# Optimization experiments

Measured on AMD Instinct MI355X. Metric: run time of the kernel, lower is better.

Reference implementation:

```python
import jax, jax.numpy as jnp
import numpy as np

B, C, H, W = 8, 512, 56, 56
CI = C // 2  # inter_channels
EPS = 1e-5   # BatchNorm eps


def setup_inputs() -> dict:
    key = jax.random.key(0)
    ks = jax.random.split(key, 11)
    s = 0.02
    return {
        "x": jax.random.normal(ks[0], (B, C, H, W), jnp.float32),
        "theta_w": jax.random.normal(ks[1], (CI, C), jnp.float32) * s,
        "theta_b": jnp.zeros((CI,), jnp.float32),
        "phi_w": jax.random.normal(ks[2], (CI, C), jnp.float32) * s,
        "phi_b": jnp.zeros((CI,), jnp.float32),
        "g_w": jax.random.normal(ks[3], (CI, C), jnp.float32) * s,
        "g_b": jnp.zeros((CI,), jnp.float32),
        "w_w": jax.random.normal(ks[4], (C, CI), jnp.float32) * s,
        "w_b": jnp.zeros((C,), jnp.float32),
        "bn_gamma": jax.random.normal(ks[5], (C,), jnp.float32) * 0.1,
        "bn_beta": jax.random.normal(ks[6], (C,), jnp.float32) * 0.1,
    }


def reference(x, theta_w, theta_b, phi_w, phi_b, g_w, g_b, w_w, w_b, bn_gamma, bn_beta):
    b, c, h, w = x.shape
    n = h * w

    def proj(wt, bi):  # 1x1 conv -> [b, out, n]
        return (jnp.einsum('bchw,oc->bohw', x, wt) + bi[None, :, None, None]).reshape(b, -1, n)

    theta_x = proj(theta_w, theta_b).transpose(0, 2, 1)  # [b, n, ci]
    phi_x = proj(phi_w, phi_b)                           # [b, ci, n]
    g_x = proj(g_w, g_b).transpose(0, 2, 1)             # [b, n, ci]

    f = jnp.einsum('bnc,bcm->bnm', theta_x, phi_x)       # [b, n, n] unscaled scores
    f_div_c = jax.nn.softmax(f, axis=-1)
    y = jnp.einsum('bnm,bmc->bnc', f_div_c, g_x)         # [b, n, ci]
    y = y.transpose(0, 2, 1).reshape(b, -1, h, w)        # [b, ci, h, w]

    w_y = jnp.einsum('bchw,oc->bohw', y, w_w) + w_b[None, :, None, None]
    # BatchNorm2d (training mode, batch statistics over B,H,W per channel)
    mean = w_y.mean(axis=(0, 2, 3))
    var = w_y.var(axis=(0, 2, 3))
    w_y = (w_y - mean[None, :, None, None]) * jax.lax.rsqrt(var[None, :, None, None] + EPS)
    w_y = w_y * bn_gamma[None, :, None, None] + bn_beta[None, :, None, None]
    return w_y + x
```

## Files before the change

### kernel.cpp

```cpp
#include <hip/hip_runtime.h>
#include <hip/hip_bf16.h>


typedef unsigned short u16;
typedef unsigned int u32;
typedef __attribute__((ext_vector_type(8))) short short8;
typedef __attribute__((ext_vector_type(4))) float floatx4;

#define B_   8
#define C_   512
#define CI_  256
#define N_   3136
#define BN_  25088

__device__ __forceinline__ u16 f2b(float f) {
    return __builtin_bit_cast(u16, __float2bfloat16(f));
}
__device__ __forceinline__ float b2f(u16 u) {
    return __bfloat162float(__builtin_bit_cast(__hip_bfloat16, u));
}
__device__ __forceinline__ floatx4 mfma16(short8 a, short8 b, floatx4 c) {
    return __builtin_amdgcn_mfma_f32_16x16x32_bf16(a, b, c, 0, 0, 0);
}
__device__ __forceinline__ void gload_lds16(const u16* g, u16* l) {
    __builtin_amdgcn_global_load_lds(
        (const __attribute__((address_space(1))) u32*)g,
        (__attribute__((address_space(3))) u32*)l, 16, 0, 0);
}

__global__ void detect_dtype(const u32* __restrict__ xw, int* __restrict__ flag,
                             float* __restrict__ stats)
{
    __shared__ int cnt;
    if (threadIdx.x == 0) cnt = 0;
    __syncthreads();
    int c = 0;
    for (int i = 0; i < 16; ++i) {
        u32 w = xw[threadIdx.x * 16 + i];
        u32 e = (w >> 7) & 0xFF;
        c += (e >= 118 && e <= 130) ? 1 : 0;
    }
    atomicAdd(&cnt, c);
    stats[threadIdx.x] = 0.f;
    stats[threadIdx.x + 256] = 0.f;
    stats[threadIdx.x + 512] = 0.f;
    stats[threadIdx.x + 768] = 0.f;
    __syncthreads();
    if (threadIdx.x == 0) *flag = (2 * cnt > 4096) ? 1 : 0;
}

__global__ __launch_bounds__(256) void convert_params(
    const void* tw, const void* tb, const void* pw, const void* pb,
    const void* gw, const void* gbi, const void* ww, const void* wb,
    const void* gamma, const void* beta,
    u16* __restrict__ dst, const int* __restrict__ flag)
{
    const void* srcs[10] = {tw, tb, pw, pb, gw, gbi, ww, wb, gamma, beta};
    const int ns[10] = {131072, 256, 131072, 256, 131072, 256, 131072, 512, 512, 512};
    int seg = blockIdx.y;
    int off = 0;
    for (int s = 0; s < 10; ++s) { if (s == seg) break; off += ns[s]; }
    const void* src = srcs[seg];
    int n = ns[seg];
    int i0 = (blockIdx.x * 256 + threadIdx.x) * 8;
    if (i0 >= n) return;
    const int fl = *flag;
    u16* d = dst + off;
    for (int k = 0; k < 8; ++k) {
        int i = i0 + k;
        if (i < n)
            d[i] = fl ? ((const u16*)src)[i] : f2b(((const float*)src)[i]);
    }
}

__global__ __launch_bounds__(256) void transpose_x(
    const void* __restrict__ in, u16* __restrict__ out,
    const int* __restrict__ flag)
{
    __shared__ u16 tile[64][68];
    const int fl = *flag;
    const int t = threadIdx.x;
    const long base = (long)blockIdx.z * (long)C_ * (long)N_;
    const int c0 = blockIdx.x * 64, r0 = blockIdx.y * 64;
    const int lr = t >> 3;
    const int lc = (t & 7) * 8;
#pragma unroll
    for (int j = 0; j < 2; ++j) {
        int rr = lr + 32 * j;
        long eoff = base + (long)(r0 + rr) * N_ + c0 + lc;
        u16 v[8] __attribute__((aligned(16)));
        if (fl) {
            const u16* pi = (const u16*)in + eoff;
            *(uint64_t*)&v[0] = *(const uint64_t*)pi;
            *(uint64_t*)&v[4] = *(const uint64_t*)(pi + 4);
        } else {
            const float* pi = (const float*)in + eoff;
            floatx4 a = *(const floatx4*)pi;
            floatx4 b4 = *(const floatx4*)(pi + 4);
#pragma unroll
            for (int k = 0; k < 4; ++k) { v[k] = f2b(a[k]); v[4 + k] = f2b(b4[k]); }
        }
        *(uint64_t*)&tile[rr][lc] = *(const uint64_t*)&v[0];
        *(uint64_t*)&tile[rr][lc + 4] = *(const uint64_t*)&v[4];
    }
    __syncthreads();
#pragma unroll
    for (int j = 0; j < 2; ++j) {
        int oc = lr + 32 * j;
        int ob = (t & 7) * 8;
        u16 vals[8] __attribute__((aligned(16)));
#pragma unroll
        for (int k = 0; k < 8; ++k) vals[k] = tile[ob + k][oc];
        u16* po = out + (long)blockIdx.z * N_ * C_ + (long)(c0 + oc) * C_ + r0 + ob;
        *(uint64_t*)po = *(const uint64_t*)vals;
        *(uint64_t*)(po + 4) = *(const uint64_t*)(vals + 4);
    }
}

__global__ __launch_bounds__(256) void transpose64(
    const u16* __restrict__ in, u16* __restrict__ out, int R, int Cc)
{
    __shared__ u16 tile[64][68];
    const int t = threadIdx.x;
    const long base = (long)blockIdx.z * (long)R * (long)Cc;
    const int c0 = blockIdx.x * 64, r0 = blockIdx.y * 64;
    const int lr = t >> 3;
    const int lc = (t & 7) * 8;
#pragma unroll
    for (int j = 0; j < 2; ++j) {
        int rr = lr + 32 * j;
        const u16* pi = in + base + (long)(r0 + rr) * Cc + c0 + lc;
        *(uint64_t*)&tile[rr][lc] = *(const uint64_t*)pi;
        *(uint64_t*)&tile[rr][lc + 4] = *(const uint64_t*)(pi + 4);
    }
    __syncthreads();
#pragma unroll
    for (int j = 0; j < 2; ++j) {
        int oc = lr + 32 * j;
        int ob = (t & 7) * 8;
        u16 vals[8] __attribute__((aligned(16)));
#pragma unroll
        for (int k = 0; k < 8; ++k) vals[k] = tile[ob + k][oc];
        u16* po = out + base + (long)(c0 + oc) * R + r0 + ob;
        *(uint64_t*)po = *(const uint64_t*)vals;
        *(uint64_t*)(po + 4) = *(const uint64_t*)(vals + 4);
    }
}

template<int K>
__global__ __launch_bounds__(256, 3) void gemm128(
    const u16* __restrict__ A,
    const u16* __restrict__ BtBase,
    const u16* __restrict__ biasBase,
    u16* __restrict__ OutBase,
    int ncols, long bstride, long ostride)
{
    __shared__ __attribute__((aligned(16))) u16 Asf[2][8][64][8];
    __shared__ __attribute__((aligned(16))) u16 Bsf[2][8][64][8];

    const int t = threadIdx.x;
    const int wave = t >> 6, lane = t & 63;
    const int q = lane >> 4, lx = lane & 15;
    const int m0 = blockIdx.x * 128;
    const int n0 = blockIdx.y * 128;
    const u16* Bt = BtBase + (long)blockIdx.z * bstride;
    const u16* bias = biasBase + (long)blockIdx.z * bstride;
    u16* Out = OutBase + (long)blockIdx.z * ostride;

    floatx4 zero4 = {0.f, 0.f, 0.f, 0.f};
    floatx4 acc[4][4];
#pragma unroll
    for (int i = 0; i < 4; ++i)
#pragma unroll
        for (int j = 0; j < 4; ++j) acc[i][j] = zero4;

    auto stage = [&](int buf, int k0) {
#pragma unroll
        for (int i = 0; i < 2; ++i) {
            int rg = wave * 2 + i;
            gload_lds16(A + (long)(m0 + rg * 16 + lx) * K + k0 + q * 8,
                        &Asf[buf][rg][0][0]);
            gload_lds16(Bt + (long)(n0 + rg * 16 + lx) * K + k0 + q * 8,
                        &Bsf[buf][rg][0][0]);
        }
    };

    stage(0, 0);
    const int rg0 = (wave >> 1) * 4, cg0 = (wave & 1) * 4;
    const int NS = K / 32;
    for (int s = 0; s < NS; ++s) {
        const int buf = s & 1;
        __syncthreads();
        if (s + 1 < NS) stage(buf ^ 1, (s + 1) * 32);
        short8 af[4], bfr[4];
#pragma unroll
        for (int i = 0; i < 4; ++i)
            af[i] = *(const short8*)&Asf[buf][rg0 + i][lane][0];
#pragma unroll
        for (int j = 0; j < 4; ++j)
            bfr[j] = *(const short8*)&Bsf[buf][cg0 + j][lane][0];
#pragma unroll
        for (int i = 0; i < 4; ++i)
#pragma unroll
            for (int j = 0; j < 4; ++j)
                acc[i][j] = mfma16(af[i], bfr[j], acc[i][j]);
    }

    const int wr = (wave >> 1) * 64, wc = (wave & 1) * 64;
#pragma unroll
    for (int j = 0; j < 4; ++j) {
        int col = n0 + wc + j * 16 + lx;
        float bv = b2f(bias[col]);
#pragma unroll
        for (int i = 0; i < 4; ++i) {
#pragma unroll
            for (int r = 0; r < 4; ++r) {
                int row = m0 + wr + i * 16 + q * 4 + r;
                Out[(long)row * ncols + col] = f2b(acc[i][j][r] + bv);
            }
        }
    }
}

__global__ __launch_bounds__(256, 2) void attn(
    const u16* __restrict__ theta,
    const u16* __restrict__ phi,
    const u16* __restrict__ gT,
    u16* __restrict__ yp0, u16* __restrict__ yp1,
    u16* __restrict__ yp2, u16* __restrict__ yp3,
    float* __restrict__ lpart)
{
    __shared__ __attribute__((aligned(16))) u16 psf[2][8][2][64][8];
    __shared__ __attribute__((aligned(16))) u16 gsf[2][16][64][8];
    __shared__ __attribute__((aligned(16))) u16 Ps[4][32][40];

    const int t = threadIdx.x;
    const int wave = t >> 6, lane = t & 63;
    const int q = lane >> 4, lx = lane & 15;
    const int b = blockIdx.y;
    const int z = blockIdx.z;
    const int n0w = blockIdx.x * 128 + wave * 32;
    const bool valid = n0w < N_;
    const u16* thb = theta + (long)b * N_ * CI_;
    const u16* phb = phi + (long)b * N_ * CI_;
    const u16* gb = gT + (long)b * CI_ * N_;

    short8 tf[2][8];
#pragma unroll
    for (int h = 0; h < 2; ++h) {
        int trow = n0w + h * 16 + lx;
        if (trow >= N_) trow = N_ - 1;
#pragma unroll
        for (int kk = 0; kk < 8; ++kk)
            tf[h][kk] = *(const short8*)(thb + (long)trow * CI_ + kk * 32 + q * 8);
    }

    floatx4 zero4 = {0.f, 0.f, 0.f, 0.f};
    floatx4 yacc[2][16];
#pragma unroll
    for (int h = 0; h < 2; ++h)
#pragma unroll
        for (int i = 0; i < 16; ++i) yacc[h][i] = zero4;
    floatx4 lacc[2] = {zero4, zero4};
    const short8 ones = {0x3F80, 0x3F80, 0x3F80, 0x3F80,
                         0x3F80, 0x3F80, 0x3F80, 0x3F80};

    const int mbeg = z * 800;
    const int mend = (z == 3) ? N_ : mbeg + 800;

    auto stage = [&](int buf, int m0) {
#pragma unroll
        for (int i = 0; i < 2; ++i) {
            int kc = wave * 2 + i;
#pragma unroll
            for (int h = 0; h < 2; ++h)
                gload_lds16(phb + (long)(m0 + h * 16 + lx) * CI_ + kc * 32 + q * 8,
                            &psf[buf][kc][h][0][0]);
        }
#pragma unroll
        for (int j4 = 0; j4 < 4; ++j4) {
            int ct = wave * 4 + j4;
            gload_lds16(gb + (long)(ct * 16 + lx) * N_ + m0 + q * 8,
                        &gsf[buf][ct][0][0]);
        }
    };

    stage(0, mbeg);
    const int NSTEP = (mend - mbeg) / 32;
    for (int s = 0; s < NSTEP; ++s) {
        const int buf = s & 1;
        __syncthreads();
        if (s + 1 < NSTEP) stage(buf ^ 1, mbeg + (s + 1) * 32);

        floatx4 sacc[2][2];
        sacc[0][0] = zero4; sacc[0][1] = zero4;
        sacc[1][0] = zero4; sacc[1][1] = zero4;
#pragma unroll
        for (int kk = 0; kk < 8; ++kk) {
            short8 bf0 = *(const short8*)&psf[buf][kk][0][lane][0];
            short8 bf1 = *(const short8*)&psf[buf][kk][1][lane][0];
            sacc[0][0] = mfma16(tf[0][kk], bf0, sacc[0][0]);
            sacc[1][0] = mfma16(tf[1][kk], bf0, sacc[1][0]);
            sacc[0][1] = mfma16(tf[0][kk], bf1, sacc[0][1]);
            sacc[1][1] = mfma16(tf[1][kk], bf1, sacc[1][1]);
        }

#pragma unroll
        for (int h = 0; h < 2; ++h)
#pragma unroll
            for (int mh = 0; mh < 2; ++mh)
#pragma unroll
                for (int r = 0; r < 4; ++r) {
                    float e = __expf(fminf(sacc[h][mh][r], 60.f));
                    Ps[wave][h * 16 + q * 4 + r][mh * 16 + lx] = f2b(e);
                }
        short8 gpre[4];
#pragma unroll
        for (int j = 0; j < 4; ++j)
            gpre[j] = *(const short8*)&gsf[buf][j][lane][0];
        __builtin_amdgcn_wave_barrier();
        short8 pA0 = *(const short8*)&Ps[wave][lx][q * 8];
        short8 pA1 = *(const short8*)&Ps[wave][16 + lx][q * 8];
        __builtin_amdgcn_wave_barrier();

#pragma unroll
        for (int j = 0; j < 4; ++j) {
            yacc[0][j] = mfma16(pA0, gpre[j], yacc[0][j]);
            yacc[1][j] = mfma16(pA1, gpre[j], yacc[1][j]);
        }
#pragma unroll
        for (int ct = 4; ct < 16; ++ct) {
            short8 gf = *(const short8*)&gsf[buf][ct][lane][0];
            yacc[0][ct] = mfma16(pA0, gf, yacc[0][ct]);
            yacc[1][ct] = mfma16(pA1, gf, yacc[1][ct]);
        }
        lacc[0] = mfma16(pA0, ones, lacc[0]);
        lacc[1] = mfma16(pA1, ones, lacc[1]);
    }

    if (valid) {
        u16* ypz = (z == 0) ? yp0 : (z == 1) ? yp1 : (z == 2) ? yp2 : yp3;
        u16* yb = ypz + (long)b * N_ * CI_;
#pragma unroll
        for (int h = 0; h < 2; ++h)
#pragma unroll
            for (int ct = 0; ct < 16; ++ct)
#pragma unroll
                for (int r = 0; r < 4; ++r)
                    yb[(long)(n0w + h * 16 + q * 4 + r) * CI_ + ct * 16 + lx] =
                        f2b(yacc[h][ct][r]);
        if (lx == 0) {
#pragma unroll
            for (int h = 0; h < 2; ++h)
#pragma unroll
                for (int r = 0; r < 4; ++r)
                    lpart[(long)z * BN_ + (long)b * N_ + n0w + h * 16 + q * 4 + r] =
                        lacc[h][r];
        }
    }
}

__global__ __launch_bounds__(256) void attn_combine(
    const u16* __restrict__ yp0, const u16* __restrict__ yp1,
    const u16* __restrict__ yp2, const u16* __restrict__ yp3,
    const float* __restrict__ lpart, u16* __restrict__ y)
{
    long tt = (long)blockIdx.x * 256 + threadIdx.x;
    long row = tt >> 5;
    int cb = (int)(tt & 31) * 8;
    float l = lpart[row] + lpart[BN_ + row] + lpart[2 * BN_ + row]
            + lpart[3 * BN_ + row];
    float rl = 1.0f / l;
    long off = row * CI_ + cb;
    short8 v0 = *(const short8*)(yp0 + off);
    short8 v1 = *(const short8*)(yp1 + off);
    short8 v2 = *(const short8*)(yp2 + off);
    short8 v3 = *(const short8*)(yp3 + off);
    u16 ov[8] __attribute__((aligned(16)));
#pragma unroll
    for (int j = 0; j < 8; ++j)
        ov[j] = f2b((b2f(((const u16*)&v0)[j]) + b2f(((const u16*)&v1)[j]) +
                     b2f(((const u16*)&v2)[j]) + b2f(((const u16*)&v3)[j])) * rl);
    *(short8*)(y + off) = *(const short8*)ov;
}

__global__ __launch_bounds__(256) void bn_stats(
    const u16* __restrict__ wy, float* __restrict__ stats)
{
    const int t = threadIdx.x;
    const long row0 = (long)blockIdx.x * 32;
    float s0 = 0.f, s1 = 0.f, q0 = 0.f, q1 = 0.f;
    for (int r = 0; r < 32; ++r) {
        const u16* p = wy + (row0 + r) * C_;
        float a = b2f(p[t]), b = b2f(p[t + 256]);
        s0 += a; q0 += a * a;
        s1 += b; q1 += b * b;
    }
    atomicAdd(&stats[t], s0);
    atomicAdd(&stats[t + 256], s1);
    atomicAdd(&stats[C_ + t], q0);
    atomicAdd(&stats[C_ + t + 256], q1);
}

__global__ __launch_bounds__(256) void bn_apply(
    const u16* __restrict__ wy, const void* __restrict__ xv,
    const u16* __restrict__ gamma, const u16* __restrict__ beta,
    const float* __restrict__ stats, void* __restrict__ outv,
    const int* __restrict__ flag)
{
    __shared__ float tile[64][65];
    const int fl = *flag;
    const int t = threadIdx.x;
    const int nb0 = blockIdx.x * 64;
    const int c0 = blockIdx.y * 64;
    const int b = blockIdx.z;
#pragma unroll
    for (int j = 0; j < 4; ++j) {
        int row = (t >> 4) + 16 * j;
        int col = (t & 15) * 4;
        const u16* p = wy + ((long)b * N_ + nb0 + row) * C_ + c0 + col;
        u16 lv[4] __attribute__((aligned(8)));
        *(uint64_t*)lv = *(const uint64_t*)p;
#pragma unroll
        for (int k = 0; k < 4; ++k) tile[row][col + k] = b2f(lv[k]);
    }
    __syncthreads();
    const float inv = 1.0f / (float)BN_;
#pragma unroll
    for (int it = 0; it < 8; ++it) {
        int oc = (t >> 5) + 8 * it;
        int on = (t & 31) * 2;
        int c = c0 + oc;
        float mean = stats[c] * inv;
        float var = stats[C_ + c] * inv - mean * mean;
        float rstd = rsqrtf(var + 1e-5f);
        float sc = b2f(gamma[c]) * rstd;
        float sh = b2f(beta[c]) - mean * sc;
        long base = ((long)b * C_ + c) * N_ + nb0 + on;
        float v0 = tile[on][oc] * sc + sh;
        float v1 = tile[on + 1][oc] * sc + sh;
        if (fl) {
            v0 += b2f(((const u16*)xv)[base]);
            v1 += b2f(((const u16*)xv)[base + 1]);
            ((u16*)outv)[base] = f2b(v0);
            ((u16*)outv)[base + 1] = f2b(v1);
        } else {
            v0 += ((const float*)xv)[base];
            v1 += ((const float*)xv)[base + 1];
            ((float*)outv)[base] = v0;
            ((float*)outv)[base + 1] = v1;
        }
    }
}

extern "C" void kernel_launch(void* const* d_in, const int* in_sizes, int n_in,
                              void* d_out, int out_size, void* d_ws, size_t ws_size,
                              hipStream_t stream)
{
    (void)in_sizes; (void)n_in; (void)out_size; (void)ws_size;

    const size_t S = 12845056;
    const size_t SE = S / 2;
    char* base = (char*)d_ws;
    u16*   xT    = (u16*)(base);
    u16*   gT    = (u16*)(base);
    u16*   y     = (u16*)(base + S);
    u16*   th    = (u16*)(base + 2 * S);
    u16*   wy    = (u16*)(base + 2 * S);
    u16*   gn    = (u16*)(base + 4 * S);
    float* lpart = (float*)(base + 5 * S);
    float* stats = (float*)(base + 5 * S + (size_t)4 * BN_ * 4);
    u16*   cw    = (u16*)(base + 5 * S + (size_t)4 * BN_ * 4 + 4096);
    int*   flag  = (int*)(base + 5 * S + (size_t)4 * BN_ * 4 + 4096 + 1055744);

    u16* ctw = cw;               u16* ctb = cw + 131072;
    u16* cww = ctb + 256 + 2 * 131328;  u16* cwb = cww + 131072;
    u16* cga = cwb + 512;        u16* cbe = cga + 512;

    u16* yp0 = (u16*)d_out;
    u16* yp1 = (u16*)d_out + SE;
    u16* yp2 = y;
    u16* yp3 = gn;

    detect_dtype<<<1, 256, 0, stream>>>((const u32*)d_in[0], flag, stats);
    convert_params<<<dim3(64, 10), 256, 0, stream>>>(
        d_in[1], d_in[2], d_in[3], d_in[4], d_in[5], d_in[6], d_in[7],
        d_in[8], d_in[9], d_in[10], cw, flag);

    transpose_x<<<dim3(N_ / 64, C_ / 64, B_), 256, 0, stream>>>(d_in[0], xT, flag);

    gemm128<C_><<<dim3(BN_ / 128, CI_ / 128, 3), 256, 0, stream>>>(
        xT, ctw, ctb, th, CI_, 131328L, (long)SE);

    transpose64<<<dim3(CI_ / 64, N_ / 64, B_), 256, 0, stream>>>(gn, gT, N_, CI_);

    attn<<<dim3(25, B_, 4), 256, 0, stream>>>(
        th, th + SE, gT, yp0, yp1, yp2, yp3, lpart);

    attn_combine<<<dim3((BN_ * 32) / 256), 256, 0, stream>>>(
        yp0, yp1, yp2, yp3, lpart, y);

    gemm128<CI_><<<dim3(BN_ / 128, C_ / 128, 1), 256, 0, stream>>>(
        y, cww, cwb, wy, C_, 0L, 0L);

    bn_stats<<<BN_ / 32, 256, 0, stream>>>(wy, stats);

    bn_apply<<<dim3(N_ / 64, C_ / 64, B_), 256, 0, stream>>>(
        wy, d_in[0], cga, cbe, stats, d_out, flag);
}
```

Before: 387.1 us.

## Fuse transpose, attention combine, and BN stats into neighbouring GEMMs; drop flag kernel

Removes the separate dtype-detect kernel by having each kernel compute the dtype flag locally from a small sample of x. Fuses the g transpose into the projection GEMM epilogue through LDS, and fuses the split-attention combine (sum of partials times 1/l) into the A-operand load of the output-projection GEMM. The batch-norm statistics are now accumulated in that GEMM's epilogue with shuffles and atomics. This cuts four kernel launches and several full-tensor round trips through memory, at the cost of register-staged A loads in gemm_w and redundant flag sampling in every block.

```diff
diff --git a/kernel.cpp b/kernel.cpp
--- a/kernel.cpp
+++ b/kernel.cpp
@@ -28,33 +28,37 @@
         (__attribute__((address_space(3))) u32*)l, 16, 0, 0);
 }
 
-__global__ void detect_dtype(const u32* __restrict__ xw, int* __restrict__ flag,
-                             float* __restrict__ stats)
-{
-    __shared__ int cnt;
-    if (threadIdx.x == 0) cnt = 0;
+__device__ __forceinline__ int block_flag(const void* x) {
+    __shared__ int cnt_;
+    if (threadIdx.x == 0) cnt_ = 0;
     __syncthreads();
+    const u32* xw = (const u32*)x;
     int c = 0;
-    for (int i = 0; i < 16; ++i) {
-        u32 w = xw[threadIdx.x * 16 + i];
+#pragma unroll
+    for (int i = 0; i < 4; ++i) {
+        u32 w = xw[threadIdx.x * 4 + i];
         u32 e = (w >> 7) & 0xFF;
         c += (e >= 118 && e <= 130) ? 1 : 0;
     }
-    atomicAdd(&cnt, c);
-    stats[threadIdx.x] = 0.f;
-    stats[threadIdx.x + 256] = 0.f;
-    stats[threadIdx.x + 512] = 0.f;
-    stats[threadIdx.x + 768] = 0.f;
+    atomicAdd(&cnt_, c);
     __syncthreads();
-    if (threadIdx.x == 0) *flag = (2 * cnt > 4096) ? 1 : 0;
+    return (2 * cnt_ > 1024) ? 1 : 0;
 }
 
 __global__ __launch_bounds__(256) void convert_params(
+    const void* __restrict__ x,
     const void* tw, const void* tb, const void* pw, const void* pb,
     const void* gw, const void* gbi, const void* ww, const void* wb,
     const void* gamma, const void* beta,
-    u16* __restrict__ dst, const int* __restrict__ flag)
-{
+    u16* __restrict__ dst, float* __restrict__ stats)
+{
+    const int fl = block_flag(x);
+    if (blockIdx.x == 0 && blockIdx.y == 0) {
+        stats[threadIdx.x] = 0.f;
+        stats[threadIdx.x + 256] = 0.f;
+        stats[threadIdx.x + 512] = 0.f;
+        stats[threadIdx.x + 768] = 0.f;
+    }
     const void* srcs[10] = {tw, tb, pw, pb, gw, gbi, ww, wb, gamma, beta};
     const int ns[10] = {131072, 256, 131072, 256, 131072, 256, 131072, 512, 512, 512};
     int seg = blockIdx.y;
@@ -64,7 +68,6 @@
     int n = ns[seg];
     int i0 = (blockIdx.x * 256 + threadIdx.x) * 8;
     if (i0 >= n) return;
-    const int fl = *flag;
     u16* d = dst + off;
     for (int k = 0; k < 8; ++k) {
         int i = i0 + k;
@@ -74,11 +77,10 @@
 }
 
 __global__ __launch_bounds__(256) void transpose_x(
-    const void* __restrict__ in, u16* __restrict__ out,
-    const int* __restrict__ flag)
-{
+    const void* __restrict__ in, u16* __restrict__ out)
+{
+    const int fl = block_flag(in);
     __shared__ u16 tile[64][68];
-    const int fl = *flag;
     const int t = threadIdx.x;
     const long base = (long)blockIdx.z * (long)C_ * (long)N_;
     const int c0 = blockIdx.x * 64, r0 = blockIdx.y * 64;
@@ -117,55 +119,25 @@
     }
 }
 
-__global__ __launch_bounds__(256) void transpose64(
-    const u16* __restrict__ in, u16* __restrict__ out, int R, int Cc)
-{
-    __shared__ u16 tile[64][68];
-    const int t = threadIdx.x;
-    const long base = (long)blockIdx.z * (long)R * (long)Cc;
-    const int c0 = blockIdx.x * 64, r0 = blockIdx.y * 64;
-    const int lr = t >> 3;
-    const int lc = (t & 7) * 8;
-#pragma unroll
-    for (int j = 0; j < 2; ++j) {
-        int rr = lr + 32 * j;
-        const u16* pi = in + base + (long)(r0 + rr) * Cc + c0 + lc;
-        *(uint64_t*)&tile[rr][lc] = *(const uint64_t*)pi;
-        *(uint64_t*)&tile[rr][lc + 4] = *(const uint64_t*)(pi + 4);
-    }
-    __syncthreads();
-#pragma unroll
-    for (int j = 0; j < 2; ++j) {
-        int oc = lr + 32 * j;
-        int ob = (t & 7) * 8;
-        u16 vals[8] __attribute__((aligned(16)));
-#pragma unroll
-        for (int k = 0; k < 8; ++k) vals[k] = tile[ob + k][oc];
-        u16* po = out + base + (long)(c0 + oc) * R + r0 + ob;
-        *(uint64_t*)po = *(const uint64_t*)vals;
-        *(uint64_t*)(po + 4) = *(const uint64_t*)(vals + 4);
-    }
-}
-
-template<int K>
-__global__ __launch_bounds__(256, 3) void gemm128(
+__global__ __launch_bounds__(256, 3) void gemm_proj(
     const u16* __restrict__ A,
     const u16* __restrict__ BtBase,
-    const u16* __restrict__ biasBase,
     u16* __restrict__ OutBase,
-    int ncols, long bstride, long ostride)
-{
-    __shared__ __attribute__((aligned(16))) u16 Asf[2][8][64][8];
-    __shared__ __attribute__((aligned(16))) u16 Bsf[2][8][64][8];
-
+    u16* __restrict__ gT,
+    long ostride)
+{
+    __shared__ __attribute__((aligned(16))) u16 smem[16896];
     const int t = threadIdx.x;
     const int wave = t >> 6, lane = t & 63;
     const int q = lane >> 4, lx = lane & 15;
     const int m0 = blockIdx.x * 128;
     const int n0 = blockIdx.y * 128;
-    const u16* Bt = BtBase + (long)blockIdx.z * bstride;
-    const u16* bias = biasBase + (long)blockIdx.z * bstride;
-    u16* Out = OutBase + (long)blockIdx.z * ostride;
+    const int zz = blockIdx.z;
+    const u16* Bt = BtBase + (long)zz * 131328L;
+    const u16* bias = Bt + 131072;
+
+    auto As = [&](int buf, int rg) -> u16* { return smem + (buf * 8 + rg) * 512; };
+    auto Bs = [&](int buf, int rg) -> u16* { return smem + 8192 + (buf * 8 + rg) * 512; };
 
     floatx4 zero4 = {0.f, 0.f, 0.f, 0.f};
     floatx4 acc[4][4];
@@ -178,27 +150,24 @@
 #pragma unroll
         for (int i = 0; i < 2; ++i) {
             int rg = wave * 2 + i;
-            gload_lds16(A + (long)(m0 + rg * 16 + lx) * K + k0 + q * 8,
-                        &Asf[buf][rg][0][0]);
-            gload_lds16(Bt + (long)(n0 + rg * 16 + lx) * K + k0 + q * 8,
-                        &Bsf[buf][rg][0][0]);
+            gload_lds16(A + (long)(m0 + rg * 16 + lx) * C_ + k0 + q * 8, As(buf, rg));
+            gload_lds16(Bt + (long)(n0 + rg * 16 + lx) * C_ + k0 + q * 8, Bs(buf, rg));
         }
     };
 
     stage(0, 0);
     const int rg0 = (wave >> 1) * 4, cg0 = (wave & 1) * 4;
-    const int NS = K / 32;
-    for (int s = 0; s < NS; ++s) {
+    for (int s = 0; s < C_ / 32; ++s) {
         const int buf = s & 1;
         __syncthreads();
-        if (s + 1 < NS) stage(buf ^ 1, (s + 1) * 32);
+        if (s + 1 < C_ / 32) stage(buf ^ 1, (s + 1) * 32);
         short8 af[4], bfr[4];
 #pragma unroll
         for (int i = 0; i < 4; ++i)
-            af[i] = *(const short8*)&Asf[buf][rg0 + i][lane][0];
+            af[i] = *(const short8*)(As(buf, rg0 + i) + lane * 8);
 #pragma unroll
         for (int j = 0; j < 4; ++j)
-            bfr[j] = *(const short8*)&Bsf[buf][cg0 + j][lane][0];
+            bfr[j] = *(const short8*)(Bs(buf, cg0 + j) + lane * 8);
 #pragma unroll
         for (int i = 0; i < 4; ++i)
 #pragma unroll
@@ -207,17 +176,47 @@
     }
 
     const int wr = (wave >> 1) * 64, wc = (wave & 1) * 64;
-#pragma unroll
-    for (int j = 0; j < 4; ++j) {
-        int col = n0 + wc + j * 16 + lx;
-        float bv = b2f(bias[col]);
-#pragma unroll
-        for (int i = 0; i < 4; ++i) {
-#pragma unroll
-            for (int r = 0; r < 4; ++r) {
-                int row = m0 + wr + i * 16 + q * 4 + r;
-                Out[(long)row * ncols + col] = f2b(acc[i][j][r] + bv);
-            }
+    if (zz < 2) {
+        u16* Out = OutBase + (long)zz * ostride;
+#pragma unroll
+        for (int j = 0; j < 4; ++j) {
+            int col = n0 + wc + j * 16 + lx;
+            float bv = b2f(bias[col]);
+#pragma unroll
+            for (int i = 0; i < 4; ++i)
+#pragma unroll
+                for (int r = 0; r < 4; ++r) {
+                    int row = m0 + wr + i * 16 + q * 4 + r;
+                    Out[(long)row * CI_ + col] = f2b(acc[i][j][r] + bv);
+                }
+        }
+    } else {
+        __syncthreads();
+#pragma unroll
+        for (int j = 0; j < 4; ++j) {
+            int cl = wc + j * 16 + lx;
+            float bv = b2f(bias[n0 + cl]);
+#pragma unroll
+            for (int i = 0; i < 4; ++i)
+#pragma unroll
+                for (int r = 0; r < 4; ++r)
+                    smem[cl * 132 + wr + i * 16 + q * 4 + r] =
+                        f2b(acc[i][j][r] + bv);
+        }
+        __syncthreads();
+#pragma unroll
+        for (int p = 0; p < 4; ++p) {
+            int cc = (t >> 3) + p * 32;
+            int nn0 = (t & 7) * 16;
+            u16 vals[16] __attribute__((aligned(16)));
+#pragma unroll
+            for (int k = 0; k < 16; ++k) vals[k] = smem[cc * 132 + nn0 + k];
+            int m = m0 + nn0;
+            int bb = m / N_;
+            int nn = m - bb * N_;
+            u16* dst = gT + ((long)bb * CI_ + (n0 + cc)) * N_ + nn;
+            *(short8*)dst = *(const short8*)&vals[0];
+            *(short8*)(dst + 8) = *(const short8*)&vals[8];
         }
     }
 }
@@ -360,56 +359,127 @@
     }
 }
 
-__global__ __launch_bounds__(256) void attn_combine(
+__global__ __launch_bounds__(256, 3) void gemm_w(
     const u16* __restrict__ yp0, const u16* __restrict__ yp1,
     const u16* __restrict__ yp2, const u16* __restrict__ yp3,
-    const float* __restrict__ lpart, u16* __restrict__ y)
-{
-    long tt = (long)blockIdx.x * 256 + threadIdx.x;
-    long row = tt >> 5;
-    int cb = (int)(tt & 31) * 8;
-    float l = lpart[row] + lpart[BN_ + row] + lpart[2 * BN_ + row]
-            + lpart[3 * BN_ + row];
-    float rl = 1.0f / l;
-    long off = row * CI_ + cb;
-    short8 v0 = *(const short8*)(yp0 + off);
-    short8 v1 = *(const short8*)(yp1 + off);
-    short8 v2 = *(const short8*)(yp2 + off);
-    short8 v3 = *(const short8*)(yp3 + off);
-    u16 ov[8] __attribute__((aligned(16)));
-#pragma unroll
-    for (int j = 0; j < 8; ++j)
-        ov[j] = f2b((b2f(((const u16*)&v0)[j]) + b2f(((const u16*)&v1)[j]) +
-                     b2f(((const u16*)&v2)[j]) + b2f(((const u16*)&v3)[j])) * rl);
-    *(short8*)(y + off) = *(const short8*)ov;
-}
-
-__global__ __launch_bounds__(256) void bn_stats(
-    const u16* __restrict__ wy, float* __restrict__ stats)
-{
+    const float* __restrict__ lpart,
+    const u16* __restrict__ Bt,
+    const u16* __restrict__ bias,
+    u16* __restrict__ wy,
+    float* __restrict__ stats)
+{
+    __shared__ __attribute__((aligned(16))) u16 Asf[2][8][64][8];
+    __shared__ __attribute__((aligned(16))) u16 Bsf[2][8][64][8];
+
     const int t = threadIdx.x;
-    const long row0 = (long)blockIdx.x * 32;
-    float s0 = 0.f, s1 = 0.f, q0 = 0.f, q1 = 0.f;
-    for (int r = 0; r < 32; ++r) {
-        const u16* p = wy + (row0 + r) * C_;
-        float a = b2f(p[t]), b = b2f(p[t + 256]);
-        s0 += a; q0 += a * a;
-        s1 += b; q1 += b * b;
-    }
-    atomicAdd(&stats[t], s0);
-    atomicAdd(&stats[t + 256], s1);
-    atomicAdd(&stats[C_ + t], q0);
-    atomicAdd(&stats[C_ + t + 256], q1);
+    const int wave = t >> 6, lane = t & 63;
+    const int q = lane >> 4, lx = lane & 15;
+    const int m0 = blockIdx.x * 128;
+    const int n0 = blockIdx.y * 128;
+
+    float rl[2];
+#pragma unroll
+    for (int i = 0; i < 2; ++i) {
+        int row = m0 + (wave * 2 + i) * 16 + lx;
+        rl[i] = 1.0f / (lpart[row] + lpart[BN_ + row] +
+                        lpart[2 * BN_ + row] + lpart[3 * BN_ + row]);
+    }
+
+    floatx4 zero4 = {0.f, 0.f, 0.f, 0.f};
+    floatx4 acc[4][4];
+#pragma unroll
+    for (int i = 0; i < 4; ++i)
+#pragma unroll
+        for (int j = 0; j < 4; ++j) acc[i][j] = zero4;
+
+    short8 va[2][4];
+    auto loadA = [&](int k0) {
+#pragma unroll
+        for (int i = 0; i < 2; ++i) {
+            long off = (long)(m0 + (wave * 2 + i) * 16 + lx) * CI_ + k0 + q * 8;
+            va[i][0] = *(const short8*)(yp0 + off);
+            va[i][1] = *(const short8*)(yp1 + off);
+            va[i][2] = *(const short8*)(yp2 + off);
+            va[i][3] = *(const short8*)(yp3 + off);
+        }
+    };
+    auto writeA = [&](int buf) {
+#pragma unroll
+        for (int i = 0; i < 2; ++i) {
+            u16 pk[8] __attribute__((aligned(16)));
+#pragma unroll
+            for (int e = 0; e < 8; ++e) {
+                float v = (b2f(((const u16*)&va[i][0])[e]) +
+                           b2f(((const u16*)&va[i][1])[e]) +
+                           b2f(((const u16*)&va[i][2])[e]) +
+                           b2f(((const u16*)&va[i][3])[e])) * rl[i];
+                pk[e] = f2b(v);
+            }
+            *(short8*)&Asf[buf][wave * 2 + i][lane][0] = *(const short8*)pk;
+        }
+    };
+    auto stageB = [&](int buf, int k0) {
+#pragma unroll
+        for (int i = 0; i < 2; ++i) {
+            int rg = wave * 2 + i;
+            gload_lds16(Bt + (long)(n0 + rg * 16 + lx) * CI_ + k0 + q * 8,
+                        &Bsf[buf][rg][0][0]);
+        }
+    };
+
+    loadA(0); writeA(0); stageB(0, 0);
+    const int rg0 = (wave >> 1) * 4, cg0 = (wave & 1) * 4;
+    const int NS = CI_ / 32;
+    for (int s = 0; s < NS; ++s) {
+        const int buf = s & 1;
+        __syncthreads();
+        if (s + 1 < NS) { loadA((s + 1) * 32); stageB(buf ^ 1, (s + 1) * 32); }
+        short8 af[4], bfr[4];
+#pragma unroll
+        for (int i = 0; i < 4; ++i)
+            af[i] = *(const short8*)&Asf[buf][rg0 + i][lane][0];
+#pragma unroll
+        for (int j = 0; j < 4; ++j)
+            bfr[j] = *(const short8*)&Bsf[buf][cg0 + j][lane][0];
+#pragma unroll
+        for (int i = 0; i < 4; ++i)
+#pragma unroll
+            for (int j = 0; j < 4; ++j)
+                acc[i][j] = mfma16(af[i], bfr[j], acc[i][j]);
+        if (s + 1 < NS) writeA(buf ^ 1);
+    }
+
+    const int wr = (wave >> 1) * 64, wc = (wave & 1) * 64;
+#pragma unroll
+    for (int j = 0; j < 4; ++j) {
+        int col = n0 + wc + j * 16 + lx;
+        float bv = b2f(bias[col]);
+        float cs = 0.f, cq = 0.f;
+#pragma unroll
+        for (int i = 0; i < 4; ++i)
+#pragma unroll
+            for (int r = 0; r < 4; ++r) {
+                int row = m0 + wr + i * 16 + q * 4 + r;
+                float v = acc[i][j][r] + bv;
+                wy[(long)row * C_ + col] = f2b(v);
+                cs += v; cq += v * v;
+            }
+        cs += __shfl_xor(cs, 16); cs += __shfl_xor(cs, 32);
+        cq += __shfl_xor(cq, 16); cq += __shfl_xor(cq, 32);
+        if (q == 0) {
+            atomicAdd(&stats[col], cs);
+            atomicAdd(&stats[C_ + col], cq);
+        }
+    }
 }
 
 __global__ __launch_bounds__(256) void bn_apply(
     const u16* __restrict__ wy, const void* __restrict__ xv,
     const u16* __restrict__ gamma, const u16* __restrict__ beta,
-    const float* __restrict__ stats, void* __restrict__ outv,
-    const int* __restrict__ flag)
-{
+    const float* __restrict__ stats, void* __restrict__ outv)
+{
+    const int fl = block_flag(xv);
     __shared__ float tile[64][65];
-    const int fl = *flag;
     const int t = threadIdx.x;
     const int nb0 = blockIdx.x * 64;
     const int c0 = blockIdx.y * 64;
@@ -463,48 +533,39 @@
     const size_t SE = S / 2;
     char* base = (char*)d_ws;
     u16*   xT    = (u16*)(base);
-    u16*   gT    = (u16*)(base);
-    u16*   y     = (u16*)(base + S);
+    u16*   yp3   = (u16*)(base);
+    u16*   yp2   = (u16*)(base + S);
     u16*   th    = (u16*)(base + 2 * S);
     u16*   wy    = (u16*)(base + 2 * S);
-    u16*   gn    = (u16*)(base + 4 * S);
+    u16*   gT    = (u16*)(base + 4 * S);
     float* lpart = (float*)(base + 5 * S);
     float* stats = (float*)(base + 5 * S + (size_t)4 * BN_ * 4);
     u16*   cw    = (u16*)(base + 5 * S + (size_t)4 * BN_ * 4 + 4096);
-    int*   flag  = (int*)(base + 5 * S + (size_t)4 * BN_ * 4 + 4096 + 1055744);
-
-    u16* ctw = cw;               u16* ctb = cw + 131072;
-    u16* cww = ctb + 256 + 2 * 131328;  u16* cwb = cww + 131072;
-    u16* cga = cwb + 512;        u16* cbe = cga + 512;
+
+    u16* ctw = cw;
+    u16* cww = cw + 393984;
+    u16* cwb = cw + 525056;
+    u16* cga = cw + 525568;
+    u16* cbe = cw + 526080;
 
     u16* yp0 = (u16*)d_out;
     u16* yp1 = (u16*)d_out + SE;
-    u16* yp2 = y;
-    u16* yp3 = gn;
-
-    detect_dtype<<<1, 256, 0, stream>>>((const u32*)d_in[0], flag, stats);
+
     convert_params<<<dim3(64, 10), 256, 0, stream>>>(
-        d_in[1], d_in[2], d_in[3], d_in[4], d_in[5], d_in[6], d_in[7],
-        d_in[8], d_in[9], d_in[10], cw, flag);
-
-    transpose_x<<<dim3(N_ / 64, C_ / 64, B_), 256, 0, stream>>>(d_in[0], xT, flag);
-
-    gemm128<C_><<<dim3(BN_ / 128, CI_ / 128, 3), 256, 0, stream>>>(
-        xT, ctw, ctb, th, CI_, 131328L, (long)SE);
-
-    transpose64<<<dim3(CI_ / 64, N_ / 64, B_), 256, 0, stream>>>(gn, gT, N_, CI_);
+        d_in[0], d_in[1], d_in[2], d_in[3], d_in[4], d_in[5], d_in[6],
+        d_in[7], d_in[8], d_in[9], d_in[10], cw, stats);
+
+    transpose_x<<<dim3(N_ / 64, C_ / 64, B_), 256, 0, stream>>>(d_in[0], xT);
+
+    gemm_proj<<<dim3(BN_ / 128, CI_ / 128, 3), 256, 0, stream>>>(
+        xT, ctw, th, gT, (long)SE);
 
     attn<<<dim3(25, B_, 4), 256, 0, stream>>>(
         th, th + SE, gT, yp0, yp1, yp2, yp3, lpart);
 
-    attn_combine<<<dim3((BN_ * 32) / 256), 256, 0, stream>>>(
-        yp0, yp1, yp2, yp3, lpart, y);
-
-    gemm128<CI_><<<dim3(BN_ / 128, C_ / 128, 1), 256, 0, stream>>>(
-        y, cww, cwb, wy, C_, 0L, 0L);
-
-    bn_stats<<<BN_ / 32, 256, 0, stream>>>(wy, stats);
+    gemm_w<<<dim3(BN_ / 128, C_ / 128), 256, 0, stream>>>(
+        yp0, yp1, yp2, yp3, lpart, cww, cwb, wy, stats);
 
     bn_apply<<<dim3(N_ / 64, C_ / 64, B_), 256, 0, stream>>>(
-        wy, d_in[0], cga, cbe, stats, d_out, flag);
-}
+        wy, d_in[0], cga, cbe, stats, d_out);
+}
```

Result: faster. 375.6 us (-3.0%).
